# Kernel optimization log

Measured on AMD Instinct MI355X. Metric: run time of the kernel, lower is better.

The kernel has to match this reference:

```python
import jax, jax.numpy as jnp
import numpy as np

NEG_BIG = -9e15  # matches torch's -9000000000000000.0 masked-fill value
ALPHA = 0.2      # LeakyReLU negative slope


def setup_inputs() -> dict:
    key = jax.random.key(0)
    k1, k2, k3, k4 = jax.random.split(key, 4)
    N, F_in, F_out = 8192, 128, 64
    h = jax.random.normal(k1, (N, F_in), dtype=jnp.float32)
    adj = jax.random.randint(k2, (N, N), 0, 2).astype(jnp.float32)
    # Glorot(gain=1.414)-scale params
    W = jax.random.normal(k3, (F_in, F_out), dtype=jnp.float32) * (1.414 * np.sqrt(2.0 / (F_in + F_out)))
    a = jax.random.normal(k4, (2 * F_out, 1), dtype=jnp.float32) * (1.414 * np.sqrt(2.0 / (2 * F_out + 1)))
    return {"h": h, "adj": adj, "W": W, "a": a}


def reference(h, adj, W, a):
    F_out = W.shape[1]
    Wh = h @ W                               # [N, F_out]
    Wh1 = Wh @ a[:F_out, :]                  # [N, 1]
    Wh2 = Wh @ a[F_out:, :]                  # [N, 1]
    e = jax.nn.leaky_relu(Wh1 + Wh2.T, negative_slope=ALPHA)  # [N, N]
    attention = jnp.where(adj > 0, e, NEG_BIG)
    attention = jax.nn.softmax(attention, axis=1)
    # dropout omitted (eval mode / p applied only in training)
    h_prime = attention @ Wh                 # [N, F_out]
    return jax.nn.elu(h_prime)               # concat=True -> ELU
```

## Files before the change

kernel.cpp:

```cpp
#include <hip/hip_runtime.h>
#include <hip/hip_bf16.h>

#define N 8192
#define FIN 128
#define FOUT 64
#define ALPHA 0.2f
#define LOG2E 1.44269504f
#define STJ 256
#define NST (N / STJ)

typedef __attribute__((ext_vector_type(8))) short short8;
typedef __attribute__((ext_vector_type(4))) float f32x4;

static __device__ __forceinline__ unsigned fkey(float x) {
    unsigned u = __float_as_uint(x);
    return (u >> 31) ? ~u : (u | 0x80000000u);
}
static __device__ __forceinline__ float fdecode(unsigned k) {
    unsigned u = (k & 0x80000000u) ? (k & 0x7FFFFFFFu) : ~k;
    return __uint_as_float(u);
}
static __device__ __forceinline__ void gll16(const float* g, float* l) {
    __builtin_amdgcn_global_load_lds(
        (const __attribute__((address_space(1))) unsigned int*)g,
        (__attribute__((address_space(3))) unsigned int*)l, 16, 0, 0);
}

__global__ __launch_bounds__(256) void k_prep(const float* __restrict__ h,
                                              const float* __restrict__ W,
                                              const float* __restrict__ a,
                                              __hip_bfloat16* __restrict__ WhB,
                                              float* __restrict__ s2,
                                              float* __restrict__ t2,
                                              unsigned* __restrict__ keys) {
    __shared__ float lH[32 * FIN];
    __shared__ float lW[FIN * FOUT];
    __shared__ float red[8];
    const int tid = threadIdx.x;
    const int c = blockIdx.x;
    const int r0 = c * 32;
    {
        const float4* src = (const float4*)(h + (size_t)r0 * FIN);
        float4* dst = (float4*)lH;
        for (int i = tid; i < 32 * FIN / 4; i += 256) dst[i] = src[i];
        const float4* ws_ = (const float4*)W;
        float4* dw = (float4*)lW;
        for (int i = tid; i < FIN * FOUT / 4; i += 256) dw[i] = ws_[i];
    }
    __syncthreads();
    const int wave = tid >> 6, lane = tid & 63;
    float acc[8] = {0.f, 0.f, 0.f, 0.f, 0.f, 0.f, 0.f, 0.f};
#pragma unroll 4
    for (int k = 0; k < FIN; ++k) {
        float wv = lW[k * FOUT + lane];
#pragma unroll
        for (int r = 0; r < 8; ++r)
            acc[r] = fmaf(lH[(wave * 8 + r) * FIN + k], wv, acc[r]);
    }
    union { unsigned short u[8]; short8 v; } frag;
#pragma unroll
    for (int e = 0; e < 8; ++e) {
        __hip_bfloat16 b = __float2bfloat16(acc[e]);
        frag.u[e] = *(unsigned short*)&b;
    }
    *(short8*)&WhB[(((size_t)c * 4 + (lane >> 4)) * 64 + (wave * 16 + (lane & 15))) * 8] = frag.v;

    const float a1 = a[lane], a2 = a[FOUT + lane];
    float smx = -1e30f, tmx = -1e30f;
#pragma unroll
    for (int r = 0; r < 8; ++r) {
        int row = r0 + wave * 8 + r;
        float sv = acc[r] * a1, tv = acc[r] * a2;
#pragma unroll
        for (int off = 32; off; off >>= 1) {
            sv += __shfl_xor(sv, off);
            tv += __shfl_xor(tv, off);
        }
        sv *= LOG2E; tv *= LOG2E;
        if (lane == 0) { s2[row] = sv; t2[row] = tv; }
        smx = fmaxf(smx, sv);
        tmx = fmaxf(tmx, tv);
    }
    if (lane == 0) { red[wave] = smx; red[4 + wave] = tmx; }
    __syncthreads();
    if (tid == 0) {
        float ms = fmaxf(fmaxf(red[0], red[1]), fmaxf(red[2], red[3]));
        float mt = fmaxf(fmaxf(red[4], red[5]), fmaxf(red[6], red[7]));
        atomicMax(keys + 0, fkey(ms));
        atomicMax(keys + 1, fkey(mt));
    }
}

__global__ __launch_bounds__(256) void k_attn(const float* __restrict__ adj,
                                              const __hip_bfloat16* __restrict__ WhB,
                                              const float* __restrict__ s2,
                                              const float* __restrict__ t2,
                                              const unsigned* __restrict__ keys,
                                              float* __restrict__ out) {
    __shared__ float bufA[3][8 * 512];
    __shared__ float sred[64];
    const int wave = threadIdx.x >> 6, lane = threadIdx.x & 63;
    const int quad = lane >> 4, l16 = lane & 15;
    const int i0 = blockIdx.x * 16;
    const int u0 = 2 * wave;

    const float sm = s2[i0 + l16];
    const float mraw = fdecode(keys[0]) + fdecode(keys[1]);
    const float mm = mraw > 0.f ? mraw : ALPHA * mraw;
    asm volatile("" :: "v"(sm), "v"(mm));
    __builtin_amdgcn_sched_barrier(0);

    const float* gawu = adj + (size_t)(i0 + l16) * N + quad * 8 + u0 * 32;
    const short8* BF = (const short8*)WhB;

    gll16(gawu,      &bufA[0][u0 * 512]);
    gll16(gawu + 4,  &bufA[0][u0 * 512 + 256]);
    gll16(gawu + 32, &bufA[0][(u0 + 1) * 512]);
    gll16(gawu + 36, &bufA[0][(u0 + 1) * 512 + 256]);
    __builtin_amdgcn_sched_barrier(0);
    size_t kc = (size_t)u0 * 4;
    short8 B0 = BF[(kc + 0) * 64 + lane];
    short8 B1 = BF[(kc + 1) * 64 + lane];
    short8 B2 = BF[(kc + 2) * 64 + lane];
    short8 B3 = BF[(kc + 3) * 64 + lane];
    short8 B4 = BF[(kc + 4) * 64 + lane];
    short8 B5 = BF[(kc + 5) * 64 + lane];
    short8 B6 = BF[(kc + 6) * 64 + lane];
    short8 B7 = BF[(kc + 7) * 64 + lane];
    const float* Tp = t2 + u0 * 32 + quad * 8;
    float4 T0 = *(const float4*)Tp;
    float4 T1 = *(const float4*)(Tp + 4);
    float4 T2v = *(const float4*)(Tp + 32);
    float4 T3v = *(const float4*)(Tp + 36);
    __builtin_amdgcn_sched_barrier(0);
    gll16(gawu + STJ,      &bufA[1][u0 * 512]);
    gll16(gawu + STJ + 4,  &bufA[1][u0 * 512 + 256]);
    gll16(gawu + STJ + 32, &bufA[1][(u0 + 1) * 512]);
    gll16(gawu + STJ + 36, &bufA[1][(u0 + 1) * 512 + 256]);
    __builtin_amdgcn_sched_barrier(0);

    f32x4 acc0 = {0,0,0,0}, acc1 = {0,0,0,0}, acc2 = {0,0,0,0}, acc3 = {0,0,0,0};
    float lsum = 0.f;
    int bi = 0;

    for (int st = 0; st < NST; ++st) {
        const bool hasN = (st + 1 < NST);
        short8 nB0, nB1, nB2, nB3, nB4, nB5, nB6, nB7;
        float4 nT0, nT1, nT2, nT3;
        if (hasN) {
            const size_t nkc = (size_t)((st + 1) * 8 + u0) * 4;
            nB0 = BF[(nkc + 0) * 64 + lane];
            nB1 = BF[(nkc + 1) * 64 + lane];
            nB2 = BF[(nkc + 2) * 64 + lane];
            nB3 = BF[(nkc + 3) * 64 + lane];
            nB4 = BF[(nkc + 4) * 64 + lane];
            nB5 = BF[(nkc + 5) * 64 + lane];
            nB6 = BF[(nkc + 6) * 64 + lane];
            nB7 = BF[(nkc + 7) * 64 + lane];
            const float* nTp = t2 + (st + 1) * STJ + u0 * 32 + quad * 8;
            nT0 = *(const float4*)nTp;
            nT1 = *(const float4*)(nTp + 4);
            nT2 = *(const float4*)(nTp + 32);
            nT3 = *(const float4*)(nTp + 36);
        }
        __builtin_amdgcn_sched_barrier(0);
        if (st + 2 < NST) {
            const float* g = gawu + (st + 2) * STJ;
            const int di = bi >= 1 ? bi - 1 : 2;
            float* d = &bufA[di][u0 * 512];
            gll16(g, d);
            gll16(g + 4, d + 256);
            gll16(g + 32, d + 512);
            gll16(g + 36, d + 768);
        }
        __builtin_amdgcn_sched_barrier(0);
        if (st < NST - 2)       asm volatile("s_waitcnt vmcnt(32)" ::: "memory");
        else if (st == NST - 2) asm volatile("s_waitcnt vmcnt(28)" ::: "memory");
        else                    asm volatile("s_waitcnt vmcnt(12)" ::: "memory");
        __builtin_amdgcn_sched_barrier(0);
#pragma unroll
        for (int uu = 0; uu < 2; ++uu) {
            const float* Au = &bufA[bi][(u0 + uu) * 512];
            float4 alo = *(const float4*)(Au + lane * 4);
            float4 ahi = *(const float4*)(Au + 256 + lane * 4);
            float4 tlo = uu ? T2v : T0;
            float4 thi = uu ? T3v : T1;
            union { __hip_bfloat162 h2[4]; short8 v; } af;
#pragma unroll
            for (int pp = 0; pp < 4; ++pp) {
                float a0 = (pp < 2) ? ((const float*)&alo)[2 * pp]     : ((const float*)&ahi)[2 * pp - 4];
                float a1 = (pp < 2) ? ((const float*)&alo)[2 * pp + 1] : ((const float*)&ahi)[2 * pp - 3];
                float t0 = (pp < 2) ? ((const float*)&tlo)[2 * pp]     : ((const float*)&thi)[2 * pp - 4];
                float t1 = (pp < 2) ? ((const float*)&tlo)[2 * pp + 1] : ((const float*)&thi)[2 * pp - 3];
                float x0 = sm + t0,                x1 = sm + t1;
                float le0 = fmaxf(x0, ALPHA * x0), le1 = fmaxf(x1, ALPHA * x1);
                float p0 = a0 * exp2f(le0 - mm),   p1 = a1 * exp2f(le1 - mm);
                __hip_bfloat162 pb = __float22bfloat162_rn(make_float2(p0, p1));
                af.h2[pp] = pb;
                lsum += __bfloat162float(pb.x) + __bfloat162float(pb.y);
            }
            if (uu == 0) {
                acc0 = __builtin_amdgcn_mfma_f32_16x16x32_bf16(af.v, B0, acc0, 0, 0, 0);
                acc1 = __builtin_amdgcn_mfma_f32_16x16x32_bf16(af.v, B1, acc1, 0, 0, 0);
                acc2 = __builtin_amdgcn_mfma_f32_16x16x32_bf16(af.v, B2, acc2, 0, 0, 0);
                acc3 = __builtin_amdgcn_mfma_f32_16x16x32_bf16(af.v, B3, acc3, 0, 0, 0);
            } else {
                acc0 = __builtin_amdgcn_mfma_f32_16x16x32_bf16(af.v, B4, acc0, 0, 0, 0);
                acc1 = __builtin_amdgcn_mfma_f32_16x16x32_bf16(af.v, B5, acc1, 0, 0, 0);
                acc2 = __builtin_amdgcn_mfma_f32_16x16x32_bf16(af.v, B6, acc2, 0, 0, 0);
                acc3 = __builtin_amdgcn_mfma_f32_16x16x32_bf16(af.v, B7, acc3, 0, 0, 0);
            }
        }
        if (hasN) {
            B0 = nB0; B1 = nB1; B2 = nB2; B3 = nB3;
            B4 = nB4; B5 = nB5; B6 = nB6; B7 = nB7;
            T0 = nT0; T1 = nT1; T2v = nT2; T3v = nT3;
        }
        bi = bi == 2 ? 0 : bi + 1;
    }

    lsum += __shfl_xor(lsum, 16);
    lsum += __shfl_xor(lsum, 32);

    float* accr = &bufA[0][0];
    *(f32x4*)&accr[((wave * 4 + 0) * 64 + lane) * 4] = acc0;
    *(f32x4*)&accr[((wave * 4 + 1) * 64 + lane) * 4] = acc1;
    *(f32x4*)&accr[((wave * 4 + 2) * 64 + lane) * 4] = acc2;
    *(f32x4*)&accr[((wave * 4 + 3) * 64 + lane) * 4] = acc3;
    if (lane < 16) sred[wave * 16 + lane] = lsum;
    __syncthreads();

    const int tile = wave;
    f32x4 tot = {0, 0, 0, 0};
#pragma unroll
    for (int w = 0; w < 4; ++w) {
        f32x4 c = *(const f32x4*)&accr[((w * 4 + tile) * 64 + lane) * 4];
        tot[0] += c[0]; tot[1] += c[1]; tot[2] += c[2]; tot[3] += c[3];
    }
#pragma unroll
    for (int r = 0; r < 4; ++r) {
        int row = quad * 4 + r;
        float lv = sred[row] + sred[16 + row] + sred[32 + row] + sred[48 + row];
        float v = tot[r] / lv;
        out[(size_t)(i0 + row) * FOUT + tile * 16 + l16] =
            v > 0.f ? v : (exp2f(v * LOG2E) - 1.f);
    }
}

extern "C" void kernel_launch(void* const* d_in, const int* in_sizes, int n_in,
                              void* d_out, int out_size, void* d_ws, size_t ws_size,
                              hipStream_t stream) {
    const float* h   = (const float*)d_in[0];
    const float* adj = (const float*)d_in[1];
    const float* W   = (const float*)d_in[2];
    const float* a   = (const float*)d_in[3];
    float* out = (float*)d_out;

    char* base = (char*)d_ws;
    __hip_bfloat16* WhB = (__hip_bfloat16*)base;     base += (size_t)N * FOUT * 2;
    float* s2 = (float*)base;                        base += (size_t)N * 4;
    float* t2 = (float*)base;                        base += (size_t)N * 4 + 1024;
    unsigned* keys = (unsigned*)base;

    hipMemsetAsync(keys, 0, 2 * sizeof(unsigned), stream);
    k_prep<<<N / 32, 256, 0, stream>>>(h, W, a, WhB, s2, t2, keys);
    k_attn<<<N / 16, 256, 0, stream>>>(adj, WhB, s2, t2, keys, out);
}
```

Baseline: 398.5 us.

## Load adjacency tiles directly into registers instead of LDS triple buffer

The adjacency stream moves from global_load_lds into a three-stage LDS ring buffer to plain float4 global loads into registers, prefetched one stage ahead. This drops the LDS round trip, the hand-tuned vmcnt waits and the scheduling barriers around the LDS copies, and shrinks shared memory so more blocks may fit per CU. In exchange the prefetch depth falls from two stages to one and register pressure rises, which may expose more memory latency on a kernel that is bound by the adjacency stream.

```diff
diff --git a/kernel.cpp b/kernel.cpp
--- a/kernel.cpp
+++ b/kernel.cpp
@@ -19,11 +19,6 @@
 static __device__ __forceinline__ float fdecode(unsigned k) {
     unsigned u = (k & 0x80000000u) ? (k & 0x7FFFFFFFu) : ~k;
     return __uint_as_float(u);
-}
-static __device__ __forceinline__ void gll16(const float* g, float* l) {
-    __builtin_amdgcn_global_load_lds(
-        (const __attribute__((address_space(1))) unsigned int*)g,
-        (__attribute__((address_space(3))) unsigned int*)l, 16, 0, 0);
 }
 
 __global__ __launch_bounds__(256) void k_prep(const float* __restrict__ h,
@@ -97,7 +92,7 @@
                                               const float* __restrict__ t2,
                                               const unsigned* __restrict__ keys,
                                               float* __restrict__ out) {
-    __shared__ float bufA[3][8 * 512];
+    __shared__ float accr[16 * 256];
     __shared__ float sred[64];
     const int wave = threadIdx.x >> 6, lane = threadIdx.x & 63;
     const int quad = lane >> 4, l16 = lane & 15;
@@ -107,47 +102,43 @@
     const float sm = s2[i0 + l16];
     const float mraw = fdecode(keys[0]) + fdecode(keys[1]);
     const float mm = mraw > 0.f ? mraw : ALPHA * mraw;
-    asm volatile("" :: "v"(sm), "v"(mm));
-    __builtin_amdgcn_sched_barrier(0);
-
-    const float* gawu = adj + (size_t)(i0 + l16) * N + quad * 8 + u0 * 32;
+
+    const float* gA = adj + (size_t)(i0 + l16) * N + quad * 8 + u0 * 32;
     const short8* BF = (const short8*)WhB;
 
-    gll16(gawu,      &bufA[0][u0 * 512]);
-    gll16(gawu + 4,  &bufA[0][u0 * 512 + 256]);
-    gll16(gawu + 32, &bufA[0][(u0 + 1) * 512]);
-    gll16(gawu + 36, &bufA[0][(u0 + 1) * 512 + 256]);
-    __builtin_amdgcn_sched_barrier(0);
-    size_t kc = (size_t)u0 * 4;
-    short8 B0 = BF[(kc + 0) * 64 + lane];
-    short8 B1 = BF[(kc + 1) * 64 + lane];
-    short8 B2 = BF[(kc + 2) * 64 + lane];
-    short8 B3 = BF[(kc + 3) * 64 + lane];
-    short8 B4 = BF[(kc + 4) * 64 + lane];
-    short8 B5 = BF[(kc + 5) * 64 + lane];
-    short8 B6 = BF[(kc + 6) * 64 + lane];
-    short8 B7 = BF[(kc + 7) * 64 + lane];
+    float4 A00 = *(const float4*)(gA);
+    float4 A01 = *(const float4*)(gA + 4);
+    float4 A10 = *(const float4*)(gA + 32);
+    float4 A11 = *(const float4*)(gA + 36);
+    const size_t kc0 = (size_t)u0 * 4;
+    short8 B0 = BF[(kc0 + 0) * 64 + lane];
+    short8 B1 = BF[(kc0 + 1) * 64 + lane];
+    short8 B2 = BF[(kc0 + 2) * 64 + lane];
+    short8 B3 = BF[(kc0 + 3) * 64 + lane];
+    short8 B4 = BF[(kc0 + 4) * 64 + lane];
+    short8 B5 = BF[(kc0 + 5) * 64 + lane];
+    short8 B6 = BF[(kc0 + 6) * 64 + lane];
+    short8 B7 = BF[(kc0 + 7) * 64 + lane];
     const float* Tp = t2 + u0 * 32 + quad * 8;
-    float4 T0 = *(const float4*)Tp;
-    float4 T1 = *(const float4*)(Tp + 4);
+    float4 T0  = *(const float4*)Tp;
+    float4 T1  = *(const float4*)(Tp + 4);
     float4 T2v = *(const float4*)(Tp + 32);
     float4 T3v = *(const float4*)(Tp + 36);
-    __builtin_amdgcn_sched_barrier(0);
-    gll16(gawu + STJ,      &bufA[1][u0 * 512]);
-    gll16(gawu + STJ + 4,  &bufA[1][u0 * 512 + 256]);
-    gll16(gawu + STJ + 32, &bufA[1][(u0 + 1) * 512]);
-    gll16(gawu + STJ + 36, &bufA[1][(u0 + 1) * 512 + 256]);
-    __builtin_amdgcn_sched_barrier(0);
 
     f32x4 acc0 = {0,0,0,0}, acc1 = {0,0,0,0}, acc2 = {0,0,0,0}, acc3 = {0,0,0,0};
     float lsum = 0.f;
-    int bi = 0;
 
     for (int st = 0; st < NST; ++st) {
         const bool hasN = (st + 1 < NST);
+        float4 nA00, nA01, nA10, nA11;
         short8 nB0, nB1, nB2, nB3, nB4, nB5, nB6, nB7;
         float4 nT0, nT1, nT2, nT3;
         if (hasN) {
+            const float* g = gA + (st + 1) * STJ;
+            nA00 = *(const float4*)(g);
+            nA01 = *(const float4*)(g + 4);
+            nA10 = *(const float4*)(g + 32);
+            nA11 = *(const float4*)(g + 36);
             const size_t nkc = (size_t)((st + 1) * 8 + u0) * 4;
             nB0 = BF[(nkc + 0) * 64 + lane];
             nB1 = BF[(nkc + 1) * 64 + lane];
@@ -164,25 +155,10 @@
             nT3 = *(const float4*)(nTp + 36);
         }
         __builtin_amdgcn_sched_barrier(0);
-        if (st + 2 < NST) {
-            const float* g = gawu + (st + 2) * STJ;
-            const int di = bi >= 1 ? bi - 1 : 2;
-            float* d = &bufA[di][u0 * 512];
-            gll16(g, d);
-            gll16(g + 4, d + 256);
-            gll16(g + 32, d + 512);
-            gll16(g + 36, d + 768);
-        }
-        __builtin_amdgcn_sched_barrier(0);
-        if (st < NST - 2)       asm volatile("s_waitcnt vmcnt(32)" ::: "memory");
-        else if (st == NST - 2) asm volatile("s_waitcnt vmcnt(28)" ::: "memory");
-        else                    asm volatile("s_waitcnt vmcnt(12)" ::: "memory");
-        __builtin_amdgcn_sched_barrier(0);
 #pragma unroll
         for (int uu = 0; uu < 2; ++uu) {
-            const float* Au = &bufA[bi][(u0 + uu) * 512];
-            float4 alo = *(const float4*)(Au + lane * 4);
-            float4 ahi = *(const float4*)(Au + 256 + lane * 4);
+            float4 alo = uu ? A10 : A00;
+            float4 ahi = uu ? A11 : A01;
             float4 tlo = uu ? T2v : T0;
             float4 thi = uu ? T3v : T1;
             union { __hip_bfloat162 h2[4]; short8 v; } af;
@@ -212,17 +188,16 @@
             }
         }
         if (hasN) {
+            A00 = nA00; A01 = nA01; A10 = nA10; A11 = nA11;
             B0 = nB0; B1 = nB1; B2 = nB2; B3 = nB3;
             B4 = nB4; B5 = nB5; B6 = nB6; B7 = nB7;
             T0 = nT0; T1 = nT1; T2v = nT2; T3v = nT3;
         }
-        bi = bi == 2 ? 0 : bi + 1;
     }
 
     lsum += __shfl_xor(lsum, 16);
     lsum += __shfl_xor(lsum, 32);
 
-    float* accr = &bufA[0][0];
     *(f32x4*)&accr[((wave * 4 + 0) * 64 + lane) * 4] = acc0;
     *(f32x4*)&accr[((wave * 4 + 1) * 64 + lane) * 4] = acc1;
     *(f32x4*)&accr[((wave * 4 + 2) * 64 + lane) * 4] = acc2;
```

Measured after the change: 393.3 us. No clear change (-1.3%).
